# Optimization experiments

Measured on AMD Instinct MI355X. Metric: run time of the kernel, lower is better.

Reference implementation:

```python
import jax, jax.numpy as jnp
import numpy as np

KH, KW = 5, 5  # kernel_size
PAD_H, PAD_W = (KH - 1) // 2, (KW - 1) // 2


def setup_inputs() -> dict:
    key = jax.random.key(0)
    x = jax.random.normal(key, (4, 3, 1024, 1024), dtype=jnp.float32)
    return {"x": x}


def reference(x):
    # x: (B, C, H, W)
    b, c, h, w = x.shape
    xr = x.reshape(b * c, 1, h, w)
    # Equivalent to the one-hot conv2d in the torch module: extract all KH*KW
    # zero-padded shifted copies -> (B*C, KH*KW, H, W)
    patches = jax.lax.conv_general_dilated_patches(
        xr,
        filter_shape=(KH, KW),
        window_strides=(1, 1),
        padding=((PAD_H, PAD_H), (PAD_W, PAD_W)),
    )
    patches = patches.reshape(b, c, KH * KW, h, w)
    # torch.median returns the lower median: (n-1)//2-th order statistic
    med_idx = (KH * KW - 1) // 2
    return jnp.sort(patches, axis=2)[:, :, med_idx]
```

## Files before the change

### kernel.cpp

```cpp
#include <hip/hip_runtime.h>


typedef __fp16 h2 __attribute__((ext_vector_type(2)));
typedef float f4v __attribute__((ext_vector_type(4)));

__device__ __forceinline__ h2 h2min(h2 a, h2 b) { return __builtin_elementwise_min(a, b); }
__device__ __forceinline__ h2 h2max(h2 a, h2 b) { return __builtin_elementwise_max(a, b); }

#define P2(a, b) { h2 _t = h2min(a, b); (b) = h2max(a, b); (a) = _t; }

template<int LO, int N, int R>
__device__ __forceinline__ void oemerge(h2* a) {
    constexpr int M = R * 2;
    if constexpr (M < N) {
        oemerge<LO, N, M>(a);
        oemerge<LO + R, N, M>(a);
#pragma unroll
        for (int i = LO + R; i + R < LO + N; i += M) P2(a[i], a[i + R]);
    } else {
        P2(a[LO], a[LO + R]);
    }
}
template<int LO, int N>
__device__ __forceinline__ void oesort(h2* a) {
    if constexpr (N > 1) {
        oesort<LO, N / 2>(a);
        oesort<LO + N / 2, N / 2>(a);
        oemerge<LO, N, 1>(a);
    }
}

#define NT 4
#define LDSW 132
#define NF2 1320

__global__ __launch_bounds__(256) void median5x5_kernel(
    const float* __restrict__ in, float* __restrict__ out, int H, int W)
{
    const int tx = threadIdx.x;
    const int ty = threadIdx.y;
    const int ch = blockIdx.z;
    const int tid = ty * 32 + tx;

    __shared__ float buf[2][20][LDSW];

    const float* img = in + (size_t)ch * H * W;
    const int bx0f = blockIdx.x * 128 - 2;
    const int by_base = blockIdx.y * (16 * NT);
    const bool x_int = (bx0f >= 0) && (bx0f + LDSW <= W);

    int gy[6], gx[6];
#pragma unroll
    for (int k = 0; k < 6; ++k) {
        const int i = tid + 256 * k;
        gy[k] = i / 66;
        gx[k] = i - gy[k] * 66;
    }
    float2 reg[6];

    auto stage_load = [&](int t) {
        const int by0 = by_base + 16 * t - 2;
#pragma unroll
        for (int k = 0; k < 6; ++k) {
            if (tid + 256 * k < NF2) {
                const int iy = by0 + gy[k];
                const bool yok = (iy >= 0) && (iy < H);
                if (x_int) {
                    const float* p = img + (size_t)iy * W + (bx0f + 2 * gx[k]);
                    reg[k] = yok ? *(const float2*)p : make_float2(0.f, 0.f);
                } else {
                    const int ix0 = bx0f + 2 * gx[k];
                    const size_t rb = (size_t)iy * W;
                    const float a = (yok && ix0 >= 0 && ix0 < W) ? img[rb + ix0] : 0.f;
                    const float b = (yok && ix0 + 1 >= 0 && ix0 + 1 < W) ? img[rb + ix0 + 1] : 0.f;
                    reg[k] = make_float2(a, b);
                }
            }
        }
    };
    auto stage_write = [&](int b) {
        float2* flat = (float2*)&buf[b][0][0];
#pragma unroll
        for (int k = 0; k < 6; ++k)
            if (tid + 256 * k < NF2) flat[tid + 256 * k] = reg[k];
    };

    stage_load(0);
    stage_write(0);
    __syncthreads();

    for (int t = 0; t < NT; ++t) {
        if (t + 1 < NT) stage_load(t + 1);

        const int cur = t & 1;
        const int r0 = 2 * ty;
        const float* tf = &buf[cur][0][0];

        h2 p[6][6];
#pragma unroll
        for (int r = 0; r < 6; ++r) {
            const float* rp = tf + (r0 + r) * LDSW + 4 * tx;
            const float4 qa = *(const float4*)rp;
            const float4 qb = *(const float4*)(rp + 4);
            const float f0 = qa.x, f1 = qa.y, f2 = qa.z, f3 = qa.w;
            const float f4 = qb.x, f5 = qb.y, f6 = qb.z, f7 = qb.w;
            p[r][0] = __builtin_amdgcn_cvt_pkrtz(f0, f2);
            p[r][1] = __builtin_amdgcn_cvt_pkrtz(f1, f3);
            p[r][2] = __builtin_amdgcn_cvt_pkrtz(f2, f4);
            p[r][3] = __builtin_amdgcn_cvt_pkrtz(f3, f5);
            p[r][4] = __builtin_amdgcn_cvt_pkrtz(f4, f6);
            p[r][5] = __builtin_amdgcn_cvt_pkrtz(f5, f7);
        }

        h2 a[16];
#pragma unroll
        for (int r = 0; r < 4; ++r)
#pragma unroll
            for (int c = 0; c < 4; ++c)
                a[r * 4 + c] = p[r + 1][c + 1];
        oesort<0, 16>(a);
        const h2* S = &a[3];

        h2 rT[4] = { p[0][1], p[0][2], p[0][3], p[0][4] };
        h2 rB[4] = { p[5][1], p[5][2], p[5][3], p[5][4] };
        h2 cL[4] = { p[1][0], p[2][0], p[3][0], p[4][0] };
        h2 cR[4] = { p[1][5], p[2][5], p[3][5], p[4][5] };
        oesort<0, 4>(rT); oesort<0, 4>(rB); oesort<0, 4>(cL); oesort<0, 4>(cR);

        h2 med[2][2];
#pragma unroll
        for (int wy = 0; wy < 2; ++wy) {
#pragma unroll
            for (int wx = 0; wx < 2; ++wx) {
                const h2* rowr = wy ? rB : rT;
                const h2* colr = wx ? cR : cL;
                h2 M[8];
#pragma unroll
                for (int i = 0; i < 4; ++i) { M[i] = rowr[i]; M[4 + i] = colr[i]; }
                oemerge<0, 8, 1>(M);
                const h2 c = p[wy ? 5 : 0][wx ? 5 : 0];

                h2 c0 = S[9];
                h2 c1 = h2max(S[8], M[0]), c2 = h2max(S[7], M[1]);
                h2 c3 = h2max(S[6], M[2]), c4 = h2max(S[5], M[3]);
                h2 c5 = h2max(S[4], M[4]), c6 = h2max(S[3], M[5]);
                h2 c7 = h2max(S[2], M[6]), c8 = h2max(S[1], M[7]);
                h2 u0 = h2min(h2min(c0, c1), h2min(c2, c3));
                h2 u1 = h2min(h2min(c4, c5), h2min(c6, c7));
                const h2 q2 = h2min(h2min(u0, u1), c8);
                h2 d0 = S[8];
                h2 d1 = h2max(S[7], M[0]), d2 = h2max(S[6], M[1]);
                h2 d3 = h2max(S[5], M[2]), d4 = h2max(S[4], M[3]);
                h2 d5 = h2max(S[3], M[4]), d6 = h2max(S[2], M[5]);
                h2 d7 = h2max(S[1], M[6]), d8 = h2max(S[0], M[7]);
                h2 w0 = h2min(h2min(d0, d1), h2min(d2, d3));
                h2 w1 = h2min(h2min(d4, d5), h2min(d6, d7));
                const h2 q1 = h2min(h2min(w0, w1), d8);
                med[wy][wx] = h2max(q1, h2min(c, q2));
            }
        }

        const int ox = blockIdx.x * 128 + 4 * tx;
        const int oy = by_base + 16 * t + r0;
        float* op = out + (size_t)ch * H * W + (size_t)oy * W + ox;
#pragma unroll
        for (int wy = 0; wy < 2; ++wy) {
            f4v o;
            o[0] = (float)med[wy][0][0];
            o[1] = (float)med[wy][1][0];
            o[2] = (float)med[wy][0][1];
            o[3] = (float)med[wy][1][1];
            __builtin_nontemporal_store(o, (f4v*)(op + (size_t)wy * W));
        }

        if (t + 1 < NT) {
            stage_write((t + 1) & 1);
            __syncthreads();
        }
    }
}

extern "C" void kernel_launch(void* const* d_in, const int* in_sizes, int n_in,
                              void* d_out, int out_size, void* d_ws, size_t ws_size,
                              hipStream_t stream) {
    const float* x = (const float*)d_in[0];
    float* out = (float*)d_out;
    const int H = 1024, W = 1024;
    const int nch = in_sizes[0] / (H * W);

    dim3 block(32, 8, 1);
    dim3 grid(W / 128, H / (16 * NT), nch);
    median5x5_kernel<<<grid, block, 0, stream>>>(x, out, H, W);
}
```

Measured before the change: 39.03 us.

## Store LDS tile as fp16 split into even/odd column planes

The shared-memory tile now holds fp16 instead of fp32. The fp32-to-fp16 conversion moves to the stage-write step, and each row is split into even and odd column halves so the compute loop can build packed pairs with shuffles instead of per-pixel conversions. Global loads now fetch 4 floats per slot with precomputed pointers, and interior blocks use an unchecked fast path. This halves LDS footprint and traffic and removes redundant conversions, in exchange for 16-bit LDS stores that may hit bank conflicts and some extra index arithmetic.

```diff
diff --git a/kernel.cpp b/kernel.cpp
--- a/kernel.cpp
+++ b/kernel.cpp
@@ -31,8 +31,9 @@
 }
 
 #define NT 4
-#define LDSW 132
-#define NF2 1320
+#define TW 132
+#define NROW 20
+#define NSLOT 660
 
 __global__ __launch_bounds__(256) void median5x5_kernel(
     const float* __restrict__ in, float* __restrict__ out, int H, int W)
@@ -42,47 +43,71 @@
     const int ch = blockIdx.z;
     const int tid = ty * 32 + tx;
 
-    __shared__ float buf[2][20][LDSW];
+    __shared__ __fp16 buf[2][NROW][TW];
 
     const float* img = in + (size_t)ch * H * W;
     const int bx0f = blockIdx.x * 128 - 2;
     const int by_base = blockIdx.y * (16 * NT);
-    const bool x_int = (bx0f >= 0) && (bx0f + LDSW <= W);
-
-    int gy[6], gx[6];
-#pragma unroll
-    for (int k = 0; k < 6; ++k) {
+    const bool x_int = (bx0f >= 0) && (bx0f + TW <= W);
+    const bool y_int = (by_base >= 2) && (by_base + 16 * NT + 2 <= H);
+    const bool fast = x_int && y_int;
+
+    int gy[3], gx[3];
+#pragma unroll
+    for (int k = 0; k < 3; ++k) {
         const int i = tid + 256 * k;
-        gy[k] = i / 66;
-        gx[k] = i - gy[k] * 66;
-    }
-    float2 reg[6];
+        gy[k] = i / 33;
+        gx[k] = i - gy[k] * 33;
+    }
+    const float* pb[3];
+#pragma unroll
+    for (int k = 0; k < 3; ++k)
+        pb[k] = img + (size_t)(by_base - 2 + gy[k]) * W + (bx0f + 4 * gx[k]);
+
+    float2 A[3], B[3];
 
     auto stage_load = [&](int t) {
-        const int by0 = by_base + 16 * t - 2;
-#pragma unroll
-        for (int k = 0; k < 6; ++k) {
-            if (tid + 256 * k < NF2) {
-                const int iy = by0 + gy[k];
-                const bool yok = (iy >= 0) && (iy < H);
-                if (x_int) {
-                    const float* p = img + (size_t)iy * W + (bx0f + 2 * gx[k]);
-                    reg[k] = yok ? *(const float2*)p : make_float2(0.f, 0.f);
-                } else {
-                    const int ix0 = bx0f + 2 * gx[k];
+        if (fast) {
+#pragma unroll
+            for (int k = 0; k < 3; ++k) {
+                if (tid + 256 * k < NSLOT) {
+                    A[k] = *(const float2*)pb[k];
+                    B[k] = *(const float2*)(pb[k] + 2);
+                    pb[k] += 16 * W;
+                }
+            }
+        } else {
+            const int by0 = by_base + 16 * t - 2;
+#pragma unroll
+            for (int k = 0; k < 3; ++k) {
+                if (tid + 256 * k < NSLOT) {
+                    const int iy = by0 + gy[k];
+                    const bool yok = (iy >= 0) && (iy < H);
                     const size_t rb = (size_t)iy * W;
-                    const float a = (yok && ix0 >= 0 && ix0 < W) ? img[rb + ix0] : 0.f;
-                    const float b = (yok && ix0 + 1 >= 0 && ix0 + 1 < W) ? img[rb + ix0 + 1] : 0.f;
-                    reg[k] = make_float2(a, b);
+                    const int c0 = bx0f + 4 * gx[k];
+                    float f[4];
+#pragma unroll
+                    for (int c = 0; c < 4; ++c) {
+                        const int ix = c0 + c;
+                        f[c] = (yok && ix >= 0 && ix < W) ? img[rb + ix] : 0.f;
+                    }
+                    A[k] = make_float2(f[0], f[1]);
+                    B[k] = make_float2(f[2], f[3]);
                 }
             }
         }
     };
     auto stage_write = [&](int b) {
-        float2* flat = (float2*)&buf[b][0][0];
-#pragma unroll
-        for (int k = 0; k < 6; ++k)
-            if (tid + 256 * k < NF2) flat[tid + 256 * k] = reg[k];
+#pragma unroll
+        for (int k = 0; k < 3; ++k) {
+            if (tid + 256 * k < NSLOT) {
+                const h2 ev = __builtin_amdgcn_cvt_pkrtz(A[k].x, B[k].x);
+                const h2 od = __builtin_amdgcn_cvt_pkrtz(A[k].y, B[k].y);
+                __fp16* rowp = &buf[b][gy[k]][0];
+                *(h2*)(rowp + 2 * gx[k]) = ev;
+                *(h2*)(rowp + 66 + 2 * gx[k]) = od;
+            }
+        }
     };
 
     stage_load(0);
@@ -94,22 +119,21 @@
 
         const int cur = t & 1;
         const int r0 = 2 * ty;
-        const float* tf = &buf[cur][0][0];
 
         h2 p[6][6];
 #pragma unroll
         for (int r = 0; r < 6; ++r) {
-            const float* rp = tf + (r0 + r) * LDSW + 4 * tx;
-            const float4 qa = *(const float4*)rp;
-            const float4 qb = *(const float4*)(rp + 4);
-            const float f0 = qa.x, f1 = qa.y, f2 = qa.z, f3 = qa.w;
-            const float f4 = qb.x, f5 = qb.y, f6 = qb.z, f7 = qb.w;
-            p[r][0] = __builtin_amdgcn_cvt_pkrtz(f0, f2);
-            p[r][1] = __builtin_amdgcn_cvt_pkrtz(f1, f3);
-            p[r][2] = __builtin_amdgcn_cvt_pkrtz(f2, f4);
-            p[r][3] = __builtin_amdgcn_cvt_pkrtz(f3, f5);
-            p[r][4] = __builtin_amdgcn_cvt_pkrtz(f4, f6);
-            p[r][5] = __builtin_amdgcn_cvt_pkrtz(f5, f7);
+            const __fp16* rp = &buf[cur][r0 + r][0];
+            const h2 a0 = *(const h2*)(rp + 2 * tx);
+            const h2 a1 = *(const h2*)(rp + 2 * tx + 2);
+            const h2 b0 = *(const h2*)(rp + 66 + 2 * tx);
+            const h2 b1 = *(const h2*)(rp + 66 + 2 * tx + 2);
+            p[r][0] = a0;
+            p[r][2] = __builtin_shufflevector(a0, a1, 1, 2);
+            p[r][4] = a1;
+            p[r][1] = b0;
+            p[r][3] = __builtin_shufflevector(b0, b1, 1, 2);
+            p[r][5] = b1;
         }
 
         h2 a[16];
```

Result: faster. 34.93 us, median of 4 (-10.5%).
